# Optimization experiments

Measured on AMD Instinct MI355X. Metric: run time of the kernel, lower is better.

## Reference

```python
import jax, jax.numpy as jnp
import numpy as np

B, S, D, H = 2, 2048, 1024, 16
HEAD_DIM = D // H  # 64


def setup_inputs() -> dict:
    key = jax.random.key(0)
    ks = jax.random.split(key, 7)
    x = jax.random.normal(ks[0], (B, S, D), dtype=jnp.float32)
    W_q = jax.random.normal(ks[1], (D, D), dtype=jnp.float32) * 0.02
    W_k = jax.random.normal(ks[2], (D, D), dtype=jnp.float32) * 0.02
    W_v = jax.random.normal(ks[3], (D, D), dtype=jnp.float32) * 0.02
    W_o = jax.random.normal(ks[4], (D, D), dtype=jnp.float32) * 0.02 / np.sqrt(2 * 12)
    b_o = jnp.zeros((D,), dtype=jnp.float32)
    # Ragged prefix attention_mask: per-row valid lengths in [S/2, S];
    # row 0 forced to full length so max_valid_len == S statically (jit-safe).
    lengths = jax.random.randint(ks[5], (B,), S // 2, S + 1)
    lengths = lengths.at[0].set(S)
    attention_mask = (jnp.arange(S)[None, :] < lengths[:, None]).astype(jnp.float32)
    return {"x": x, "attention_mask": attention_mask, "W_q": W_q, "W_k": W_k,
            "W_v": W_v, "W_o": W_o, "b_o": b_o}


def reference(x, attention_mask, W_q, W_k, W_v, W_o, b_o):
    b, s, d = x.shape
    h, hd = H, HEAD_DIM
    # QKV projections (no bias, qkv_bias=False)
    q = (x @ W_q.T).reshape(b, s, h, hd).transpose(0, 2, 1, 3)  # [b,h,s,hd]
    # Masking keys/values at invalid (padded) positions; for prefix masks this
    # is exactly the module's per-batch packing loop (max_valid_len == s).
    m = attention_mask[:, None, :, None]  # [b,1,s,1]
    k = ((x @ W_k.T).reshape(b, s, h, hd).transpose(0, 2, 1, 3)) * m
    v = ((x @ W_v.T).reshape(b, s, h, hd).transpose(0, 2, 1, 3)) * m
    # Naive causal attention, same op order as the torch module:
    # mask with -inf first, then scale by 1/sqrt(head_dim), then softmax.
    causal = jnp.triu(jnp.ones((s, s), dtype=bool), 1)  # True above diagonal
    scores = jnp.einsum('bhqd,bhkd->bhqk', q, k)
    scores = jnp.where(causal[None, None], -jnp.inf, scores)
    att = jax.nn.softmax(scores / jnp.sqrt(jnp.float32(hd)), axis=-1)
    ctx = jnp.einsum('bhqk,bhkd->bhqd', att, v)  # [b,h,s,hd]
    ctx = ctx.transpose(0, 2, 1, 3).reshape(b, s, d)
    # Output projection (dropout is inference no-op)
    return ctx @ W_o.T + b_o
```

## Files before the change

kernel.cpp:

```cpp
#include <hip/hip_runtime.h>

#define B_  2
#define S_  2048
#define D_  1024
#define H_  16
#define HD_ 64
#define N3_ 3072
#define M_  4096

typedef _Float16 f16;
typedef _Float16 f16x2 __attribute__((ext_vector_type(2)));
typedef _Float16 f16x4 __attribute__((ext_vector_type(4)));
typedef _Float16 f16x8 __attribute__((ext_vector_type(8)));
typedef float    f32x4 __attribute__((ext_vector_type(4)));

__device__ __forceinline__ void async16(const f16* g, f16* l) {
  __builtin_amdgcn_global_load_lds(
      (const __attribute__((address_space(1))) unsigned int*)g,
      (__attribute__((address_space(3))) unsigned int*)l, 16, 0, 0);
}

__device__ __forceinline__ f16x2 pkrtz(float a, float b) {
  return __builtin_bit_cast(f16x2, __builtin_amdgcn_cvt_pkrtz(a, b));
}

__global__ __launch_bounds__(256)
void cvt_all(const float* __restrict__ x,
             const float* __restrict__ Wq, const float* __restrict__ Wk,
             const float* __restrict__ Wv, const float* __restrict__ Wo,
             f16* __restrict__ xb, f16* __restrict__ wdst, float qscale) {
  const int i = blockIdx.x * 256 + threadIdx.x;
  const int XN4 = M_ * D_ / 4;
  const int WN4 = D_ * D_ / 4;
  const float* src;
  f16* dst;
  float scale = 1.0f;
  int j;
  if (i < XN4) {
    src = x; dst = xb; j = i;
  } else {
    int k = i - XN4;
    int m = k >> 18;
    j = k & (WN4 - 1);
    src = (m == 0) ? Wq : (m == 1) ? Wk : (m == 2) ? Wv : Wo;
    if (m == 0) scale = qscale;
    dst = wdst + (size_t)m * D_ * D_;
  }
  float4 v = ((const float4*)src)[j];
  f16x4 o = { (f16)(v.x * scale), (f16)(v.y * scale),
              (f16)(v.z * scale), (f16)(v.w * scale) };
  ((f16x4*)dst)[j] = o;
}

__global__ __launch_bounds__(256)
void gemm_qkv(const f16* __restrict__ A, const f16* __restrict__ Bw,
              f16* __restrict__ Cq, f16* __restrict__ vtout,
              const float* __restrict__ mask) {
  __shared__ f16 As[128 * 64];
  __shared__ f16 Bs[128 * 64];

  const int tid  = threadIdx.x;
  const int lane = tid & 63;
  const int w    = tid >> 6;
  const int lcol = lane & 15;
  const int quad = lane >> 4;
  const int lx   = lcol & 7;
  const int wave_m = w >> 1, wave_n = w & 1;

  const int m0 = blockIdx.y * 128;
  const int n0 = blockIdx.x * 128;

  const int rr  = lane >> 3;
  const int gch = (lane & 7) ^ rr;

  const f16* gA[4];
  const f16* gB[4];
  f16* lA[4];
  f16* lB[4];
#pragma unroll
  for (int i = 0; i < 4; i++) {
    int seg = i * 4 + w;
    int row = seg * 8 + rr;
    gA[i] = A  + (size_t)(m0 + row) * D_ + gch * 8;
    gB[i] = Bw + (size_t)(n0 + row) * D_ + gch * 8;
    lA[i] = As + seg * 512;
    lB[i] = Bs + seg * 512;
  }

  int offA[4], offB[4];
#pragma unroll
  for (int i = 0; i < 4; i++) {
    offA[i] = (wave_m * 64 + i * 16 + lcol) * 64;
    offB[i] = (wave_n * 64 + i * 16 + lcol) * 64;
  }

  const f32x4 zero = {0.f, 0.f, 0.f, 0.f};
  f32x4 acc[4][4];
#pragma unroll
  for (int i = 0; i < 4; i++)
#pragma unroll
    for (int j = 0; j < 4; j++) acc[i][j] = zero;

  for (int k0 = 0; k0 < D_; k0 += 64) {
    __syncthreads();
#pragma unroll
    for (int i = 0; i < 4; i++) async16(gA[i] + k0, lA[i]);
#pragma unroll
    for (int i = 0; i < 4; i++) async16(gB[i] + k0, lB[i]);
    __syncthreads();

#pragma unroll
    for (int ks = 0; ks < 2; ks++) {
      const int co = ((quad + 4 * ks) ^ lx) * 8;
      f16x8 af[4], bf[4];
#pragma unroll
      for (int i = 0; i < 4; i++) af[i] = *(const f16x8*)(As + offA[i] + co);
#pragma unroll
      for (int i = 0; i < 4; i++) bf[i] = *(const f16x8*)(Bs + offB[i] + co);
#pragma unroll
      for (int mi = 0; mi < 4; mi++)
#pragma unroll
        for (int ni = 0; ni < 4; ni++)
          acc[mi][ni] = __builtin_amdgcn_mfma_f32_16x16x32_f16(
              af[mi], bf[ni], acc[mi][ni], 0, 0, 0);
    }
  }

  if (n0 >= 2 * D_) {
#pragma unroll
    for (int mi = 0; mi < 4; mi++) {
      const int mgb = m0 + wave_m * 64 + mi * 16 + quad * 4;
      const int b = mgb >> 11, s = mgb & (S_ - 1);
      const float mk0 = mask[mgb], mk1 = mask[mgb + 1];
      const float mk2 = mask[mgb + 2], mk3 = mask[mgb + 3];
#pragma unroll
      for (int ni = 0; ni < 4; ni++) {
        const int vcol = n0 - 2 * D_ + wave_n * 64 + ni * 16 + lcol;
        f16x4 v = { (f16)(acc[mi][ni][0] * mk0), (f16)(acc[mi][ni][1] * mk1),
                    (f16)(acc[mi][ni][2] * mk2), (f16)(acc[mi][ni][3] * mk3) };
        *(f16x4*)(vtout +
                  ((size_t)(b * 16 + (vcol >> 6)) * 64 + (vcol & 63)) * S_ + s) = v;
      }
    }
  } else {
    const bool kmask = (n0 >= D_);
#pragma unroll
    for (int mi = 0; mi < 4; mi++) {
#pragma unroll
      for (int r = 0; r < 4; r++) {
        int mg = m0 + wave_m * 64 + mi * 16 + quad * 4 + r;
        float mk = kmask ? mask[mg] : 1.0f;
#pragma unroll
        for (int ni = 0; ni < 4; ni++) {
          int ng = n0 + wave_n * 64 + ni * 16 + lcol;
          Cq[(size_t)mg * N3_ + ng] = (f16)(acc[mi][ni][r] * mk);
        }
      }
    }
  }
}

__global__ __launch_bounds__(256)
void gemm_proj(const f16* __restrict__ A, const f16* __restrict__ Bw,
               float* __restrict__ Cf, const float* __restrict__ bias) {
  __shared__ f16 As[64 * 64];
  __shared__ f16 Bs[128 * 64];

  const int tid  = threadIdx.x;
  const int lane = tid & 63;
  const int w    = tid >> 6;
  const int lcol = lane & 15;
  const int quad = lane >> 4;
  const int lx   = lcol & 7;
  const int wave_m = w >> 1, wave_n = w & 1;

  const int m0 = blockIdx.y * 64;
  const int n0 = blockIdx.x * 128;

  const int rr  = lane >> 3;
  const int gch = (lane & 7) ^ rr;

  const f16* gA[2];
  const f16* gB[4];
  f16* lA[2];
  f16* lB[4];
#pragma unroll
  for (int i = 0; i < 2; i++) {
    int seg = 2 * w + i;
    gA[i] = A + (size_t)(m0 + seg * 8 + rr) * D_ + gch * 8;
    lA[i] = As + seg * 512;
  }
#pragma unroll
  for (int i = 0; i < 4; i++) {
    int seg = i * 4 + w;
    gB[i] = Bw + (size_t)(n0 + seg * 8 + rr) * D_ + gch * 8;
    lB[i] = Bs + seg * 512;
  }

  int offA[2], offB[4];
#pragma unroll
  for (int i = 0; i < 2; i++) offA[i] = (wave_m * 32 + i * 16 + lcol) * 64;
#pragma unroll
  for (int i = 0; i < 4; i++) offB[i] = (wave_n * 64 + i * 16 + lcol) * 64;

  const f32x4 zero = {0.f, 0.f, 0.f, 0.f};
  f32x4 acc[2][4];
#pragma unroll
  for (int i = 0; i < 2; i++)
#pragma unroll
    for (int j = 0; j < 4; j++) acc[i][j] = zero;

  for (int k0 = 0; k0 < D_; k0 += 64) {
    __syncthreads();
#pragma unroll
    for (int i = 0; i < 2; i++) async16(gA[i] + k0, lA[i]);
#pragma unroll
    for (int i = 0; i < 4; i++) async16(gB[i] + k0, lB[i]);
    __syncthreads();

#pragma unroll
    for (int ks = 0; ks < 2; ks++) {
      const int co = ((quad + 4 * ks) ^ lx) * 8;
      f16x8 af[2], bf[4];
#pragma unroll
      for (int i = 0; i < 2; i++) af[i] = *(const f16x8*)(As + offA[i] + co);
#pragma unroll
      for (int i = 0; i < 4; i++) bf[i] = *(const f16x8*)(Bs + offB[i] + co);
#pragma unroll
      for (int mi = 0; mi < 2; mi++)
#pragma unroll
        for (int ni = 0; ni < 4; ni++)
          acc[mi][ni] = __builtin_amdgcn_mfma_f32_16x16x32_f16(
              af[mi], bf[ni], acc[mi][ni], 0, 0, 0);
    }
  }

#pragma unroll
  for (int mi = 0; mi < 2; mi++) {
#pragma unroll
    for (int r = 0; r < 4; r++) {
      int mg = m0 + wave_m * 32 + mi * 16 + quad * 4 + r;
#pragma unroll
      for (int ni = 0; ni < 4; ni++) {
        int ng = n0 + wave_n * 64 + ni * 16 + lcol;
        Cf[(size_t)mg * D_ + ng] = acc[mi][ni][r] + bias[ng];
      }
    }
  }
}

__global__ __launch_bounds__(256)
void flash_attn7(const f16* __restrict__ qkv, const f16* __restrict__ vt,
                 f16* __restrict__ ctx, float* __restrict__ part) {
  __shared__ f16 Ks[64 * 64];
  __shared__ f16 Vs[64 * 64];

  const int tid  = threadIdx.x;
  const int lane = tid & 63;
  const int w    = tid >> 6;
  const int lcol = lane & 15;
  const int quad = lane >> 4;
  const int lx   = lcol & 7;

  const int id   = blockIdx.x;
  const int bh   = (id & 7) + 8 * ((id >> 3) & 3);
  const int u    = id >> 5;
  const int p    = u & 15;
  const int role = u >> 4;
  const int g    = 31 - p;
  const int b    = bh >> 4, h = bh & 15;

  const int rsub  = lane >> 3;
  const int gch   = (lane & 7) ^ rsub;
  const int krow0 = w * 8 + rsub;
  const int krow1 = 32 + w * 8 + rsub;
  const f16* Kg = qkv + (size_t)b * S_ * N3_ + D_ + h * HD_;
  const f16* Vg = vt + (size_t)bh * HD_ * S_;
  f16* ldsK0 = Ks + (w * 8) * 64;
  f16* ldsK1 = Ks + (32 + w * 8) * 64;
  f16* ldsV0 = Vs + (w * 8) * 64;
  f16* ldsV1 = Vs + (32 + w * 8) * 64;

  const f32x4 zero = {0.f, 0.f, 0.f, 0.f};
  f32x4 o[4];
  float lp;

  auto run = [&](int qt, int ktb, int kte) {
    const int qrow = qt * 64 + w * 16 + lcol;
    const f16* Qp  = qkv + (size_t)(b * S_ + qrow) * N3_ + h * HD_;
    const f16x8 qb0 = *(const f16x8*)(Qp + quad * 8);
    const f16x8 qb1 = *(const f16x8*)(Qp + 32 + quad * 8);
#pragma unroll
    for (int i = 0; i < 4; i++) o[i] = zero;
    lp = 0.f;

    for (int kt = ktb; kt < kte; kt++) {
      const int kbase = kt * 64;
      __syncthreads();
      async16(Kg + (size_t)(kbase + krow0) * N3_ + gch * 8, ldsK0);
      async16(Kg + (size_t)(kbase + krow1) * N3_ + gch * 8, ldsK1);
      async16(Vg + (size_t)krow0 * S_ + kbase + gch * 8, ldsV0);
      async16(Vg + (size_t)krow1 * S_ + kbase + gch * 8, ldsV1);
      __syncthreads();

      f32x4 sc[4];
#pragma unroll
      for (int ct = 0; ct < 4; ct++) {
        const f16* kr = Ks + (ct * 16 + lcol) * 64;
        f16x8 kf0 = *(const f16x8*)(kr + ((quad    ) ^ lx) * 8);
        f16x8 kf1 = *(const f16x8*)(kr + ((quad + 4) ^ lx) * 8);
        f32x4 z = zero;
        z = __builtin_amdgcn_mfma_f32_16x16x32_f16(kf0, qb0, z, 0, 0, 0);
        z = __builtin_amdgcn_mfma_f32_16x16x32_f16(kf1, qb1, z, 0, 0, 0);
        sc[ct] = z;
      }

      if (kt == qt) {
#pragma unroll
        for (int ct = 0; ct < 4; ct++) {
          int koff = ct * 16 + quad * 4;
          int qoff = w * 16 + lcol;
#pragma unroll
          for (int r = 0; r < 4; r++)
            if (koff + r > qoff) sc[ct][r] = -1e30f;
        }
      }

      f16x4 pf[4];
#pragma unroll
      for (int ct = 0; ct < 4; ct++) {
        float e0 = exp2f(sc[ct][0]);
        float e1 = exp2f(sc[ct][1]);
        float e2 = exp2f(sc[ct][2]);
        float e3 = exp2f(sc[ct][3]);
        lp += (e0 + e1) + (e2 + e3);
        f16x2 lo = pkrtz(e0, e1);
        f16x2 hi = pkrtz(e2, e3);
        f16x4 pv = { lo[0], lo[1], hi[0], hi[1] };
        pf[ct] = pv;
      }

#pragma unroll
      for (int ht = 0; ht < 4; ht++) {
        const f16* vr = Vs + (ht * 16 + lcol) * 64 + (quad & 1) * 4;
#pragma unroll
        for (int ct = 0; ct < 4; ct++) {
          f16x4 vf = *(const f16x4*)(vr + (((2 * ct + (quad >> 1)) ^ lx) * 8));
          o[ht] = __builtin_amdgcn_mfma_f32_16x16x16f16(vf, pf[ct], o[ht], 0, 0, 0);
        }
      }
    }
    lp += __shfl_xor(lp, 16);
    lp += __shfl_xor(lp, 32);
  };

  if (role == 0) {
    run(g, 0, 16);
    float* slot = part + ((size_t)(bh * 16 + p) * 2 + 0) * 4160;
#pragma unroll
    for (int ht = 0; ht < 4; ht++)
      *(f32x4*)(slot + (w * 16 + lcol) * 64 + ht * 16 + quad * 4) = o[ht];
    if (quad == 0) slot[4096 + w * 16 + lcol] = lp;
  } else {
    run(g, 16, g + 1);
    float* slot = part + ((size_t)(bh * 16 + p) * 2 + 1) * 4160;
#pragma unroll
    for (int ht = 0; ht < 4; ht++)
      *(f32x4*)(slot + (w * 16 + lcol) * 64 + ht * 16 + quad * 4) = o[ht];
    if (quad == 0) slot[4096 + w * 16 + lcol] = lp;

    run(p, 0, p + 1);
    const float inv = 1.f / lp;
    const int qrow = p * 64 + w * 16 + lcol;
    f16* cp = ctx + (size_t)(b * S_ + qrow) * D_ + h * HD_ + quad * 4;
#pragma unroll
    for (int ht = 0; ht < 4; ht++) {
      f16x4 ov = { (f16)(o[ht][0] * inv), (f16)(o[ht][1] * inv),
                   (f16)(o[ht][2] * inv), (f16)(o[ht][3] * inv) };
      *(f16x4*)(cp + ht * 16) = ov;
    }
  }
}

__global__ __launch_bounds__(256)
void attn_combine(const float* __restrict__ part, f16* __restrict__ ctx) {
  const int sid = blockIdx.x;
  const int bh  = sid >> 4, p = sid & 15;
  const int g   = 31 - p;
  const int b   = bh >> 4, h = bh & 15;
  const int t   = threadIdx.x;
  const int row = t >> 2;
  const int c0  = (t & 3) * 16;

  const float* sA = part + ((size_t)sid * 2 + 0) * 4160;
  const float* sB = part + ((size_t)sid * 2 + 1) * 4160;
  const float inv = 1.f / (sA[4096 + row] + sB[4096 + row]);
  const int qrow = g * 64 + row;
  f16* cp = ctx + (size_t)(b * S_ + qrow) * D_ + h * HD_ + c0;
#pragma unroll
  for (int j0 = 0; j0 < 16; j0 += 4) {
    f32x4 a  = *(const f32x4*)(sA + row * 64 + c0 + j0);
    f32x4 bb = *(const f32x4*)(sB + row * 64 + c0 + j0);
    f16x4 ov = { (f16)((a[0] + bb[0]) * inv), (f16)((a[1] + bb[1]) * inv),
                 (f16)((a[2] + bb[2]) * inv), (f16)((a[3] + bb[3]) * inv) };
    *(f16x4*)(cp + j0) = ov;
  }
}

extern "C" void kernel_launch(void* const* d_in, const int* in_sizes, int n_in,
                              void* d_out, int out_size, void* d_ws, size_t ws_size,
                              hipStream_t stream) {
  (void)in_sizes; (void)n_in; (void)out_size; (void)ws_size;
  const float* x  = (const float*)d_in[0];
  const float* am = (const float*)d_in[1];
  const float* Wq = (const float*)d_in[2];
  const float* Wk = (const float*)d_in[3];
  const float* Wv = (const float*)d_in[4];
  const float* Wo = (const float*)d_in[5];
  const float* bo = (const float*)d_in[6];
  float* out = (float*)d_out;

  f16* ws   = (f16*)d_ws;
  f16* wqkv = ws;
  f16* wo16 = wqkv + (size_t)3 * D_ * D_;
  f16* xb   = wo16 + (size_t)D_ * D_;
  f16* qkvb = xb + (size_t)M_ * D_;
  f16* vtb  = qkvb + (size_t)M_ * N3_;
  f16* ctxb = vtb + (size_t)M_ * D_;
  float* part = (float*)(ctxb + (size_t)M_ * D_);

  const float qscale = 0.125f * 1.4426950408889634f;

  cvt_all<<<dim3((M_ * D_ + 4 * D_ * D_) / 1024), 256, 0, stream>>>(
      x, Wq, Wk, Wv, Wo, xb, wqkv, qscale);

  gemm_qkv<<<dim3(N3_ / 128, M_ / 128), 256, 0, stream>>>(
      xb, wqkv, qkvb, vtb, am);
  flash_attn7<<<dim3(1024), 256, 0, stream>>>(qkvb, vtb, ctxb, part);
  attn_combine<<<dim3(512), 256, 0, stream>>>(part, ctxb);
  gemm_proj<<<dim3(D_ / 128, M_ / 64), 256, 0, stream>>>(
      ctxb, wo16, out, bo);
}
```

Baseline: 188.0 us.

## Use two waves per attention block, each handling 32 query rows

The flash attention kernel now runs two waves of 128 threads instead of four. Each wave processes two 16-row query sub-tiles, so every K and V fragment read from LDS feeds twice as many MFMAs. This halves LDS read traffic per unit of compute and raises instruction-level parallelism. Each thread issues more async loads, and exp2f is replaced with raw v_exp_f32 inline asm. In exchange, register pressure per wave rises and there are fewer waves per block to hide latency.

New measurement: 180.8 us. 3.8% less time.

```diff
diff --git a/kernel.cpp b/kernel.cpp
--- a/kernel.cpp
+++ b/kernel.cpp
@@ -22,6 +22,10 @@
 
 __device__ __forceinline__ f16x2 pkrtz(float a, float b) {
   return __builtin_bit_cast(f16x2, __builtin_amdgcn_cvt_pkrtz(a, b));
+}
+
+__device__ __forceinline__ float vexp2(float x) {
+  float r; asm("v_exp_f32 %0, %1" : "=v"(r) : "v"(x)); return r;
 }
 
 __global__ __launch_bounds__(256)
@@ -249,8 +253,8 @@
   }
 }
 
-__global__ __launch_bounds__(256)
-void flash_attn7(const f16* __restrict__ qkv, const f16* __restrict__ vt,
+__global__ __launch_bounds__(128)
+void flash_attn8(const f16* __restrict__ qkv, const f16* __restrict__ vt,
                  f16* __restrict__ ctx, float* __restrict__ part) {
   __shared__ f16 Ks[64 * 64];
   __shared__ f16 Vs[64 * 64];
@@ -270,74 +274,96 @@
   const int g    = 31 - p;
   const int b    = bh >> 4, h = bh & 15;
 
-  const int rsub  = lane >> 3;
-  const int gch   = (lane & 7) ^ rsub;
-  const int krow0 = w * 8 + rsub;
-  const int krow1 = 32 + w * 8 + rsub;
+  const int rsub = lane >> 3;
+  const int gch  = (lane & 7) ^ rsub;
   const f16* Kg = qkv + (size_t)b * S_ * N3_ + D_ + h * HD_;
   const f16* Vg = vt + (size_t)bh * HD_ * S_;
-  f16* ldsK0 = Ks + (w * 8) * 64;
-  f16* ldsK1 = Ks + (32 + w * 8) * 64;
-  f16* ldsV0 = Vs + (w * 8) * 64;
-  f16* ldsV1 = Vs + (32 + w * 8) * 64;
+
+  int srow[4];
+  f16 *ldsK[4], *ldsV[4];
+#pragma unroll
+  for (int i = 0; i < 4; i++) {
+    const int r0 = w * 32 + i * 8;
+    srow[i] = r0 + rsub;
+    ldsK[i] = Ks + r0 * 64;
+    ldsV[i] = Vs + r0 * 64;
+  }
 
   const f32x4 zero = {0.f, 0.f, 0.f, 0.f};
-  f32x4 o[4];
-  float lp;
+  f32x4 o0[4], o1[4];
+  float lp0, lp1;
 
   auto run = [&](int qt, int ktb, int kte) {
-    const int qrow = qt * 64 + w * 16 + lcol;
-    const f16* Qp  = qkv + (size_t)(b * S_ + qrow) * N3_ + h * HD_;
-    const f16x8 qb0 = *(const f16x8*)(Qp + quad * 8);
-    const f16x8 qb1 = *(const f16x8*)(Qp + 32 + quad * 8);
-#pragma unroll
-    for (int i = 0; i < 4; i++) o[i] = zero;
-    lp = 0.f;
+    const int qrow0 = qt * 64 + w * 32 + lcol;
+    const int qrow1 = qrow0 + 16;
+    const f16* Qp0 = qkv + (size_t)(b * S_ + qrow0) * N3_ + h * HD_;
+    const f16* Qp1 = qkv + (size_t)(b * S_ + qrow1) * N3_ + h * HD_;
+    const f16x8 qa0 = *(const f16x8*)(Qp0 + quad * 8);
+    const f16x8 qa1 = *(const f16x8*)(Qp0 + 32 + quad * 8);
+    const f16x8 qb0 = *(const f16x8*)(Qp1 + quad * 8);
+    const f16x8 qb1 = *(const f16x8*)(Qp1 + 32 + quad * 8);
+#pragma unroll
+    for (int i = 0; i < 4; i++) { o0[i] = zero; o1[i] = zero; }
+    lp0 = 0.f; lp1 = 0.f;
 
     for (int kt = ktb; kt < kte; kt++) {
       const int kbase = kt * 64;
       __syncthreads();
-      async16(Kg + (size_t)(kbase + krow0) * N3_ + gch * 8, ldsK0);
-      async16(Kg + (size_t)(kbase + krow1) * N3_ + gch * 8, ldsK1);
-      async16(Vg + (size_t)krow0 * S_ + kbase + gch * 8, ldsV0);
-      async16(Vg + (size_t)krow1 * S_ + kbase + gch * 8, ldsV1);
+#pragma unroll
+      for (int i = 0; i < 4; i++)
+        async16(Kg + (size_t)(kbase + srow[i]) * N3_ + gch * 8, ldsK[i]);
+#pragma unroll
+      for (int i = 0; i < 4; i++)
+        async16(Vg + (size_t)srow[i] * S_ + kbase + gch * 8, ldsV[i]);
       __syncthreads();
 
-      f32x4 sc[4];
+      f32x4 sc0[4], sc1[4];
 #pragma unroll
       for (int ct = 0; ct < 4; ct++) {
         const f16* kr = Ks + (ct * 16 + lcol) * 64;
         f16x8 kf0 = *(const f16x8*)(kr + ((quad    ) ^ lx) * 8);
         f16x8 kf1 = *(const f16x8*)(kr + ((quad + 4) ^ lx) * 8);
-        f32x4 z = zero;
-        z = __builtin_amdgcn_mfma_f32_16x16x32_f16(kf0, qb0, z, 0, 0, 0);
-        z = __builtin_amdgcn_mfma_f32_16x16x32_f16(kf1, qb1, z, 0, 0, 0);
-        sc[ct] = z;
+        f32x4 z0 = zero;
+        z0 = __builtin_amdgcn_mfma_f32_16x16x32_f16(kf0, qa0, z0, 0, 0, 0);
+        z0 = __builtin_amdgcn_mfma_f32_16x16x32_f16(kf1, qa1, z0, 0, 0, 0);
+        sc0[ct] = z0;
+        f32x4 z1 = zero;
+        z1 = __builtin_amdgcn_mfma_f32_16x16x32_f16(kf0, qb0, z1, 0, 0, 0);
+        z1 = __builtin_amdgcn_mfma_f32_16x16x32_f16(kf1, qb1, z1, 0, 0, 0);
+        sc1[ct] = z1;
       }
 
       if (kt == qt) {
+        const int qoff0 = w * 32 + lcol;
+        const int qoff1 = qoff0 + 16;
 #pragma unroll
         for (int ct = 0; ct < 4; ct++) {
-          int koff = ct * 16 + quad * 4;
-          int qoff = w * 16 + lcol;
-#pragma unroll
-          for (int r = 0; r < 4; r++)
-            if (koff + r > qoff) sc[ct][r] = -1e30f;
+          const int koff = ct * 16 + quad * 4;
+#pragma unroll
+          for (int r = 0; r < 4; r++) {
+            if (koff + r > qoff0) sc0[ct][r] = -1e30f;
+            if (koff + r > qoff1) sc1[ct][r] = -1e30f;
+          }
         }
       }
 
-      f16x4 pf[4];
+      f16x4 pf0[4], pf1[4];
 #pragma unroll
       for (int ct = 0; ct < 4; ct++) {
-        float e0 = exp2f(sc[ct][0]);
-        float e1 = exp2f(sc[ct][1]);
-        float e2 = exp2f(sc[ct][2]);
-        float e3 = exp2f(sc[ct][3]);
-        lp += (e0 + e1) + (e2 + e3);
-        f16x2 lo = pkrtz(e0, e1);
-        f16x2 hi = pkrtz(e2, e3);
-        f16x4 pv = { lo[0], lo[1], hi[0], hi[1] };
-        pf[ct] = pv;
+        float a0 = vexp2(sc0[ct][0]), a1 = vexp2(sc0[ct][1]);
+        float a2 = vexp2(sc0[ct][2]), a3 = vexp2(sc0[ct][3]);
+        lp0 += (a0 + a1) + (a2 + a3);
+        f16x2 alo = pkrtz(a0, a1);
+        f16x2 ahi = pkrtz(a2, a3);
+        f16x4 pa = { alo[0], alo[1], ahi[0], ahi[1] };
+        pf0[ct] = pa;
+        float b0 = vexp2(sc1[ct][0]), b1 = vexp2(sc1[ct][1]);
+        float b2 = vexp2(sc1[ct][2]), b3 = vexp2(sc1[ct][3]);
+        lp1 += (b0 + b1) + (b2 + b3);
+        f16x2 blo = pkrtz(b0, b1);
+        f16x2 bhi = pkrtz(b2, b3);
+        f16x4 pb = { blo[0], blo[1], bhi[0], bhi[1] };
+        pf1[ct] = pb;
       }
 
 #pragma unroll
@@ -346,38 +372,58 @@
 #pragma unroll
         for (int ct = 0; ct < 4; ct++) {
           f16x4 vf = *(const f16x4*)(vr + (((2 * ct + (quad >> 1)) ^ lx) * 8));
-          o[ht] = __builtin_amdgcn_mfma_f32_16x16x16f16(vf, pf[ct], o[ht], 0, 0, 0);
+          o0[ht] = __builtin_amdgcn_mfma_f32_16x16x16f16(vf, pf0[ct], o0[ht], 0, 0, 0);
+          o1[ht] = __builtin_amdgcn_mfma_f32_16x16x16f16(vf, pf1[ct], o1[ht], 0, 0, 0);
         }
       }
     }
-    lp += __shfl_xor(lp, 16);
-    lp += __shfl_xor(lp, 32);
+    lp0 += __shfl_xor(lp0, 16);
+    lp0 += __shfl_xor(lp0, 32);
+    lp1 += __shfl_xor(lp1, 16);
+    lp1 += __shfl_xor(lp1, 32);
   };
+
+  const int row0 = w * 32 + lcol;
+  const int row1 = row0 + 16;
 
   if (role == 0) {
     run(g, 0, 16);
     float* slot = part + ((size_t)(bh * 16 + p) * 2 + 0) * 4160;
 #pragma unroll
-    for (int ht = 0; ht < 4; ht++)
-      *(f32x4*)(slot + (w * 16 + lcol) * 64 + ht * 16 + quad * 4) = o[ht];
-    if (quad == 0) slot[4096 + w * 16 + lcol] = lp;
+    for (int ht = 0; ht < 4; ht++) {
+      *(f32x4*)(slot + row0 * 64 + ht * 16 + quad * 4) = o0[ht];
+      *(f32x4*)(slot + row1 * 64 + ht * 16 + quad * 4) = o1[ht];
+    }
+    if (quad == 0) {
+      slot[4096 + row0] = lp0;
+      slot[4096 + row1] = lp1;
+    }
   } else {
     run(g, 16, g + 1);
     float* slot = part + ((size_t)(bh * 16 + p) * 2 + 1) * 4160;
 #pragma unroll
-    for (int ht = 0; ht < 4; ht++)
-      *(f32x4*)(slot + (w * 16 + lcol) * 64 + ht * 16 + quad * 4) = o[ht];
-    if (quad == 0) slot[4096 + w * 16 + lcol] = lp;
+    for (int ht = 0; ht < 4; ht++) {
+      *(f32x4*)(slot + row0 * 64 + ht * 16 + quad * 4) = o0[ht];
+      *(f32x4*)(slot + row1 * 64 + ht * 16 + quad * 4) = o1[ht];
+    }
+    if (quad == 0) {
+      slot[4096 + row0] = lp0;
+      slot[4096 + row1] = lp1;
+    }
 
     run(p, 0, p + 1);
-    const float inv = 1.f / lp;
-    const int qrow = p * 64 + w * 16 + lcol;
-    f16* cp = ctx + (size_t)(b * S_ + qrow) * D_ + h * HD_ + quad * 4;
+    const float inv0 = 1.f / lp0;
+    const float inv1 = 1.f / lp1;
+    f16* cp0 = ctx + (size_t)(b * S_ + p * 64 + row0) * D_ + h * HD_ + quad * 4;
+    f16* cp1 = ctx + (size_t)(b * S_ + p * 64 + row1) * D_ + h * HD_ + quad * 4;
 #pragma unroll
     for (int ht = 0; ht < 4; ht++) {
-      f16x4 ov = { (f16)(o[ht][0] * inv), (f16)(o[ht][1] * inv),
-                   (f16)(o[ht][2] * inv), (f16)(o[ht][3] * inv) };
-      *(f16x4*)(cp + ht * 16) = ov;
+      f16x4 ov0 = { (f16)(o0[ht][0] * inv0), (f16)(o0[ht][1] * inv0),
+                    (f16)(o0[ht][2] * inv0), (f16)(o0[ht][3] * inv0) };
+      *(f16x4*)(cp0 + ht * 16) = ov0;
+      f16x4 ov1 = { (f16)(o1[ht][0] * inv1), (f16)(o1[ht][1] * inv1),
+                    (f16)(o1[ht][2] * inv1), (f16)(o1[ht][3] * inv1) };
+      *(f16x4*)(cp1 + ht * 16) = ov1;
     }
   }
 }
@@ -436,7 +482,7 @@
 
   gemm_qkv<<<dim3(N3_ / 128, M_ / 128), 256, 0, stream>>>(
       xb, wqkv, qkvb, vtb, am);
-  flash_attn7<<<dim3(1024), 256, 0, stream>>>(qkvb, vtb, ctxb, part);
+  flash_attn8<<<dim3(1024), 128, 0, stream>>>(qkvb, vtb, ctxb, part);
   attn_combine<<<dim3(512), 256, 0, stream>>>(part, ctxb);
   gemm_proj<<<dim3(D_ / 128, M_ / 64), 256, 0, stream>>>(
       ctxb, wo16, out, bo);
```
